# Performance work log

Measured on AMD Instinct MI355X. Metric: run time of the kernel, lower is better.

## Reference

```python
import jax, jax.numpy as jnp
import numpy as np

EPS_N = 1e-12   # F.normalize eps
LN_EPS = 1e-5   # LayerNorm eps
N_NODES = 20000
NODES_PER_GRAPH = 200
DEG = 8
N_EDGES = N_NODES * DEG
F_NODE = 36
F_EDGE = 10
HID = 128
HEAD = 8
DK = HID // HEAD
G = N_NODES // NODES_PER_GRAPH


def l2norm(x):
    n = jnp.sqrt(jnp.sum(x * x, axis=-1, keepdims=True))
    return x / jnp.maximum(n, EPS_N)


def layer_norm(x, g, b):
    m = jnp.mean(x, axis=-1, keepdims=True)
    v = jnp.mean((x - m) ** 2, axis=-1, keepdims=True)
    return (x - m) / jnp.sqrt(v + LN_EPS) * g + b


def seg_softmax(e, idx, n):
    m = jax.ops.segment_max(e, idx, num_segments=n)
    ex = jnp.exp(e - m[idx])
    s = jax.ops.segment_sum(ex, idx, num_segments=n)
    return ex / s[idx]


def sfe_conv(x, src, dst, eattr, We, Wq, Wk, Wv, Wo, bo, g, b):
    # x: [N, in], src/dst: [Ef] (self loops included), eattr: [Ef, F_EDGE]
    n = x.shape[0]
    emb = l2norm(eattr @ We)                  # edge_encoder + F.normalize
    xj = x[src] + emb                          # source node + edge embedding
    q = (xj @ Wq).reshape(-1, HEAD, DK)
    ksum = (x[dst] @ Wk).reshape(-1, HEAD, DK).sum(axis=1)  # sum over k-heads (matmul+sum in source)
    v = (xj @ Wv).reshape(-1, HEAD, DK)
    energy = jnp.einsum('ehd,ed->eh', q, ksum) / jnp.sqrt(jnp.float32(HID))
    att = seg_softmax(energy, dst, n)          # segment softmax over target nodes, per head
    msg = (v * att[:, :, None]).reshape(-1, HID)
    agg = jax.ops.segment_sum(msg, dst, num_segments=n)
    y = layer_norm(agg @ Wo + bo, g, b)        # update(): out_norm(out_linear(.))
    return layer_norm(y, g, b)                 # forward() applies out_norm again


def setup_inputs():
    key = jax.random.key(0)
    ks = jax.random.split(key, 16)
    x = jax.random.normal(ks[0], (N_NODES, F_NODE), jnp.float32)
    edge_attr = jax.random.uniform(ks[1], (N_EDGES, F_EDGE), jnp.float32)
    src = jnp.repeat(jnp.arange(N_NODES), DEG)
    base = src - src % NODES_PER_GRAPH
    off = jax.random.randint(ks[2], (N_EDGES,), 1, NODES_PER_GRAPH)
    dst = base + (src % NODES_PER_GRAPH + off) % NODES_PER_GRAPH  # same-graph, no self loops
    edge_index = jnp.stack([src, dst]).astype(jnp.int64)
    batch = (jnp.arange(N_NODES) // NODES_PER_GRAPH).astype(jnp.int64)
    interface_pos = jnp.arange(0, N_NODES, 2, dtype=jnp.int64)
    s = lambda k, sh: jax.random.normal(k, sh, jnp.float32) * 0.05
    return dict(
        x=x, edge_attr=edge_attr,
        c0_We=s(ks[3], (F_EDGE, F_NODE)), c0_Wq=s(ks[4], (F_NODE, HID)),
        c0_Wk=s(ks[5], (F_NODE, HID)), c0_Wv=s(ks[6], (F_NODE, HID)),
        c0_Wo=s(ks[7], (HID, HID)), c0_bo=jnp.zeros((HID,), jnp.float32),
        c0_g=jnp.ones((HID,), jnp.float32), c0_b=jnp.zeros((HID,), jnp.float32),
        cs_We=s(ks[8], (2, F_EDGE, HID)), cs_Wq=s(ks[9], (2, HID, HID)),
        cs_Wk=s(ks[10], (2, HID, HID)), cs_Wv=s(ks[11], (2, HID, HID)),
        cs_Wo=s(ks[12], (2, HID, HID)), cs_bo=jnp.zeros((2, HID), jnp.float32),
        cs_g=jnp.ones((2, HID), jnp.float32), cs_b=jnp.zeros((2, HID), jnp.float32),
        gate=s(ks[13], (HID,)), W1=s(ks[14], (HID, HID // 2)),
        b1=jnp.zeros((HID // 2,), jnp.float32), W2=s(ks[15], (HID // 2, 1)),
        b2=jnp.zeros((1,), jnp.float32),
        edge_index=edge_index, batch=batch, interface_pos=interface_pos,
        graph_num=G)


def reference(x, edge_attr, c0_We, c0_Wq, c0_Wk, c0_Wv, c0_Wo, c0_bo, c0_g, c0_b,
              cs_We, cs_Wq, cs_Wk, cs_Wv, cs_Wo, cs_bo, cs_g, cs_b,
              gate, W1, b1, W2, b2, edge_index, batch, interface_pos, graph_num):
    n = x.shape[0]
    loops = jnp.arange(n)
    src = jnp.concatenate([edge_index[0], loops])
    dst = jnp.concatenate([edge_index[1], loops])
    ea = jnp.concatenate([l2norm(edge_attr),
                          jnp.zeros((n, edge_attr.shape[1]), edge_attr.dtype)])
    h = l2norm(x)
    h = jnp.tanh(sfe_conv(h, src, dst, ea, c0_We, c0_Wq, c0_Wk, c0_Wv, c0_Wo, c0_bo, c0_g, c0_b))
    for i in range(cs_We.shape[0]):
        h = jnp.tanh(sfe_conv(h, src, dst, ea, cs_We[i], cs_Wq[i], cs_Wk[i], cs_Wv[i],
                              cs_Wo[i], cs_bo[i], cs_g[i], cs_b[i]))
    # global self-attention pooling over interface nodes, per graph
    xi = h[interface_pos]
    bi = batch[interface_pos]
    att = seg_softmax(xi @ gate, bi, graph_num)
    pooled = jax.ops.segment_sum(att[:, None] * xi, bi, num_segments=graph_num)  # [G, HID]
    out = jnp.tanh(pooled @ W1 + b1)
    return jax.nn.sigmoid(out @ W2 + b2)  # [G, 1]
```

## Files before the change

### kernel.cpp

```cpp
#include <hip/hip_runtime.h>
#include <math.h>

#define HID 128
#define HEAD 8
#define DK 16
#define FEDGE 10
#define FNODE 36
#define ESCALE 0.08838834764831845f
#define CH 32

typedef float f32x4v __attribute__((ext_vector_type(4)));
typedef short bf16x8 __attribute__((ext_vector_type(8)));

struct PackArgs {
  const float* src[8];
  unsigned short* dst[8];
  int fin[8];
  int kt[8];
  int blk_off[8];
};

struct PrepArgs {
  const float* We[3];
  const float* Wq[3];
  const float* Wk[3];
  const float* Wv[3];
  float* C[3];
  float* WeWv[3];
  float* Gram[3];
  float* Wksum[3];
  int fin[3];
};

__device__ __forceinline__ void fma4(float4& z, float s, const float4& w) {
  z.x += s * w.x;
  z.y += s * w.y;
  z.z += s * w.z;
  z.w += s * w.w;
}

__device__ __forceinline__ unsigned short f2bf(float f) {
  unsigned int u = __float_as_uint(f);
  u += 0x7fffu + ((u >> 16) & 1u);
  return (unsigned short)(u >> 16);
}

__device__ __forceinline__ void store_bf8(unsigned short* p, float4 a, float4 b) {
  uint4 u;
  u.x = (unsigned)f2bf(a.x) | ((unsigned)f2bf(a.y) << 16);
  u.y = (unsigned)f2bf(a.z) | ((unsigned)f2bf(a.w) << 16);
  u.z = (unsigned)f2bf(b.x) | ((unsigned)f2bf(b.y) << 16);
  u.w = (unsigned)f2bf(b.z) | ((unsigned)f2bf(b.w) << 16);
  *(uint4*)p = u;
}

__global__ void k_zero_i(int* __restrict__ p, int n) {
  int i = blockIdx.x * 256 + threadIdx.x;
  if (i < n) p[i] = 0;
}

__global__ void k_count(const int* __restrict__ ei, int E, int* __restrict__ cnt) {
  int e = blockIdx.x * 256 + threadIdx.x;
  if (e >= E) return;
  atomicAdd(&cnt[ei[E + e]], 1);
}

__global__ __launch_bounds__(1024) void k_scan(const int* __restrict__ cnt, int* __restrict__ off,
                                               int* __restrict__ cur, int* __restrict__ scsr_s,
                                               int n, int total) {
  __shared__ int s[1024];
  int t = threadIdx.x;
  const int C = (n + 1023) / 1024;
  int local[32];
  int base = t * C;
  int sum = 0;
  for (int j = 0; j < C; ++j) {
    int i = base + j;
    int v = (i < n) ? cnt[i] : 0;
    local[j] = sum;
    sum += v;
  }
  s[t] = sum;
  __syncthreads();
  for (int dd = 1; dd < 1024; dd <<= 1) {
    int v = (t >= dd) ? s[t - dd] : 0;
    __syncthreads();
    s[t] += v;
    __syncthreads();
  }
  int excl = (t == 0) ? 0 : s[t - 1];
  for (int j = 0; j < C; ++j) {
    int i = base + j;
    if (i < n) {
      int o = excl + local[j];
      off[i] = o;
      cur[i] = o;
      scsr_s[o + i] = i;
    }
  }
  if (t == 0) off[n] = total;
}

__global__ void k_fill(const int* __restrict__ ei, int E, int* __restrict__ cur,
                       int* __restrict__ scsr_s, int* __restrict__ pmap) {
  int e = blockIdx.x * 256 + threadIdx.x;
  if (e >= E) return;
  int t = ei[E + e];
  int pos = atomicAdd(&cur[t], 1) + t + 1;
  pmap[e] = pos;
  scsr_s[pos] = ei[e];
}

__global__ __launch_bounds__(128) void k_wprep3(PrepArgs a) {
  int l = blockIdx.x / FEDGE, t = blockIdx.x - l * FEDGE;
  int d = threadIdx.x;
  int fin = a.fin[l];
  const float* We = a.We[l];
  const float* Wq = a.Wq[l];
  const float* Wk = a.Wk[l];
  const float* Wv = a.Wv[l];
  __shared__ float sw[HID];
  if (d < fin) sw[d] = We[t * fin + d];
  __syncthreads();
  float c = 0.f, wv = 0.f;
  for (int i = 0; i < fin; ++i) {
    c += sw[i] * Wq[i * HID + d];
    wv += sw[i] * Wv[i * HID + d];
  }
  a.C[l][t * HID + d] = c;
  a.WeWv[l][t * HID + d] = wv;
  if (d < FEDGE) {
    float g = 0.f;
    for (int i = 0; i < fin; ++i) g += sw[i] * We[d * fin + i];
    a.Gram[l][t * FEDGE + d] = g;
  }
  for (int r = t; r < fin; r += FEDGE) {
    if (d < DK) {
      float s = 0.f;
#pragma unroll
      for (int hh = 0; hh < HEAD; ++hh) s += Wk[r * HID + hh * DK + d];
      a.Wksum[l][r * DK + d] = s;
    }
  }
}

__global__ __launch_bounds__(64) void k_wpack8(PackArgs pa) {
  int b = blockIdx.x, lane = threadIdx.x;
  int m = 0;
#pragma unroll
  for (int i = 1; i < 8; ++i) m += (b >= pa.blk_off[i]);
  int local = b - pa.blk_off[m];
  int KT = pa.kt[m];
  int ct = local / KT, kt = local - ct * KT;
  const float* W = pa.src[m];
  int fin = pa.fin[m];
  int col = ct * 16 + (lane & 15);
  int kbase = kt * 32 + (lane >> 4) * 8;
  float v[8];
#pragma unroll
  for (int j = 0; j < 8; ++j) {
    int k = kbase + j;
    v[j] = (k < fin) ? W[k * HID + col] : 0.f;
  }
  store_bf8(pa.dst[m] + (size_t)local * 512 + lane * 8, make_float4(v[0], v[1], v[2], v[3]),
            make_float4(v[4], v[5], v[6], v[7]));
}

__global__ void k_l2e_sea(const float* __restrict__ eattr, const int* __restrict__ pmap,
                          const float* __restrict__ Gram3, float* __restrict__ sea3, int E,
                          int ET) {
  int e = blockIdx.x * 256 + threadIdx.x;
  if (e >= E) return;
  float a[FEDGE];
  float ss = 0.f;
  for (int i = 0; i < FEDGE; ++i) {
    a[i] = eattr[(size_t)e * FEDGE + i];
    ss += a[i] * a[i];
  }
  float s0 = 1.f / fmaxf(sqrtf(ss), 1e-12f);
  for (int i = 0; i < FEDGE; ++i) a[i] *= s0;
  int pos = pmap[e];
  for (int l = 0; l < 3; ++l) {
    const float* G = Gram3 + l * FEDGE * FEDGE;
    float gp = 0.f;
#pragma unroll
    for (int j = 0; j < FEDGE; ++j) {
      float t = 0.f;
#pragma unroll
      for (int u = 0; u < FEDGE; ++u) t += G[j * FEDGE + u] * a[u];
      gp += t * a[j];
    }
    float scl = 1.f / fmaxf(sqrtf(gp), 1e-12f);
    float* sp = sea3 + (size_t)l * ET * FEDGE + (size_t)pos * FEDGE;
#pragma unroll
    for (int u = 0; u < FEDGE; ++u) sp[u] = scl * a[u];
  }
}

__global__ __launch_bounds__(256) void k1_l2x(
    const float* __restrict__ x, const unsigned short* __restrict__ qpack,
    const unsigned short* __restrict__ vpack, const float* __restrict__ Wksum,
    const float* __restrict__ C, const int* __restrict__ off, float* __restrict__ qx,
    float* __restrict__ kb, float* __restrict__ vxb, float* __restrict__ Mout,
    float* __restrict__ energy_csr, int N) {
  const int fin = FNODE;
  int d = threadIdx.x;
  int n0 = blockIdx.x * 16;
  int nb = min(16, N - n0);
  __shared__ __align__(16) float sx[16][40];
  __shared__ __align__(16) unsigned short afrag[2][64][8];
  __shared__ float sk[16][DK];
  {
    int col = d & 127, h2 = d >> 7;
#pragma unroll
    for (int rr = 0; rr < 8; ++rr) {
      int r = h2 * 8 + rr;
      if (col < fin) sx[r][col] = (r < nb) ? x[(size_t)(n0 + r) * fin + col] : 0.f;
    }
  }
  __syncthreads();
  int grp = d >> 4, j16 = d & 15;
  {
    float ssq = 0.f;
    for (int i = j16; i < fin; i += 16) ssq += sx[grp][i] * sx[grp][i];
#pragma unroll
    for (int o = 8; o; o >>= 1) ssq += __shfl_xor(ssq, o, 16);
    float scl = 1.f / fmaxf(sqrtf(ssq), 1e-12f);
    for (int i = j16; i < fin; i += 16) sx[grp][i] *= scl;
  }
  __syncthreads();
  int lane = d & 63, wvid = d >> 6;
  if (d < 128) {
    int kt = d >> 6;
    int m = lane & 15, k0 = kt * 32 + (lane >> 4) * 8;
    float v[8];
#pragma unroll
    for (int j = 0; j < 8; ++j) {
      int k = k0 + j;
      v[j] = (k < fin) ? sx[m][k] : 0.f;
    }
    store_bf8(&afrag[kt][lane][0], make_float4(v[0], v[1], v[2], v[3]),
              make_float4(v[4], v[5], v[6], v[7]));
  }
  {
    float kk = 0.f;
    for (int i = 0; i < fin; ++i) kk += sx[grp][i] * Wksum[i * DK + j16];
    sk[grp][j16] = kk;
    if (grp < nb) kb[(size_t)(n0 + grp) * DK + j16] = kk;
  }
  __syncthreads();
  int colD = lane & 15, quad = lane >> 4;
#pragma unroll
  for (int t = 0; t < 4; ++t) {
    int g = wvid * 4 + t;
    int mat = g >> 3, ct = g & 7;
    const unsigned short* P = mat ? vpack : qpack;
    f32x4v acc = {0.f, 0.f, 0.f, 0.f};
#pragma unroll
    for (int kt = 0; kt < 2; ++kt) {
      bf16x8 a = *(const bf16x8*)&afrag[kt][lane][0];
      bf16x8 b = *(const bf16x8*)(P + ((size_t)(ct * 2 + kt) * 64 + lane) * 8);
      acc = __builtin_amdgcn_mfma_f32_16x16x32_bf16(a, b, acc, 0, 0, 0);
    }
    float* out = mat ? vxb : qx;
#pragma unroll
    for (int reg = 0; reg < 4; ++reg) {
      int node = quad * 4 + reg;
      if (node < nb) out[(size_t)(n0 + node) * HID + ct * 16 + colD] = acc[reg];
    }
  }
  __syncthreads();
  if (d < 128) {
    int n = d >> 3, h = d & 7;
    if (n < nb) {
      const float* qp = qx + (size_t)(n0 + n) * HID + h * DK;
      float e = 0.f;
#pragma unroll
      for (int j = 0; j < DK; ++j) e += qp[j] * sk[n][j];
      int nn = n0 + n;
      energy_csr[(size_t)(off[nn] + nn) * HEAD + h] = e * ESCALE;
    }
  }
  if (d < HEAD * FEDGE) {
    int hh = d / FEDGE, tt = d - hh * FEDGE;
    float crow[16];
    *(float4*)&crow[0] = *(const float4*)&C[tt * HID + hh * DK + 0];
    *(float4*)&crow[4] = *(const float4*)&C[tt * HID + hh * DK + 4];
    *(float4*)&crow[8] = *(const float4*)&C[tt * HID + hh * DK + 8];
    *(float4*)&crow[12] = *(const float4*)&C[tt * HID + hh * DK + 12];
    for (int r = 0; r < nb; ++r) {
      float m = 0.f;
#pragma unroll
      for (int j = 0; j < DK; ++j) m += sk[r][j] * crow[j];
      Mout[((size_t)(n0 + r) * HEAD + hh) * 16 + tt] = m;
    }
  }
}

__global__ __launch_bounds__(256) void k_post_k1(
    const float* agg, const unsigned short* __restrict__ opack, const float* __restrict__ bo,
    const float* __restrict__ gg, const float* __restrict__ bb,
    const unsigned short* __restrict__ qpack, const unsigned short* __restrict__ vpack,
    const float* __restrict__ Wksum, const float* __restrict__ C, const int* __restrict__ off,
    float* qx, float* __restrict__ kb, float* __restrict__ vxb, float* __restrict__ Mout,
    float* __restrict__ energy_csr, int N) {
  int d = threadIdx.x;
  int n0 = blockIdx.x * 16;
  int nb = min(16, N - n0);
  __shared__ __align__(16) unsigned short afrag[4][64][8];
  __shared__ __align__(16) float sz[16][132];
  __shared__ __align__(16) unsigned short hfrag[4][64][8];
  __shared__ float sk[16][DK];
  int lane = d & 63, wvid = d >> 6;
  {
    int kt = wvid;
    int m = lane & 15, k0 = kt * 32 + (lane >> 4) * 8;
    const float* p = agg + (size_t)(n0 + m) * HID + k0;
    float4 x0 = *(const float4*)p;
    float4 x1 = *(const float4*)(p + 4);
    store_bf8(&afrag[kt][lane][0], x0, x1);
  }
  __syncthreads();
  int colD = lane & 15, quad = lane >> 4;
  {
    int ct0 = wvid * 2, ct1 = wvid * 2 + 1;
    float bias0 = bo[ct0 * 16 + colD], bias1 = bo[ct1 * 16 + colD];
    f32x4v acc0 = {bias0, bias0, bias0, bias0};
    f32x4v acc1 = {bias1, bias1, bias1, bias1};
#pragma unroll
    for (int kt = 0; kt < 4; ++kt) {
      bf16x8 a = *(const bf16x8*)&afrag[kt][lane][0];
      bf16x8 b0 = *(const bf16x8*)(opack + ((size_t)(ct0 * 4 + kt) * 64 + lane) * 8);
      bf16x8 b1 = *(const bf16x8*)(opack + ((size_t)(ct1 * 4 + kt) * 64 + lane) * 8);
      acc0 = __builtin_amdgcn_mfma_f32_16x16x32_bf16(a, b0, acc0, 0, 0, 0);
      acc1 = __builtin_amdgcn_mfma_f32_16x16x32_bf16(a, b1, acc1, 0, 0, 0);
    }
#pragma unroll
    for (int reg = 0; reg < 4; ++reg) {
      int node = quad * 4 + reg;
      sz[node][ct0 * 16 + colD] = acc0[reg];
      sz[node][ct1 * 16 + colD] = acc1[reg];
    }
  }
  __syncthreads();
  {
    int c4 = d & 31, rs = d >> 5;
    int col0 = c4 * 4, r0 = rs * 2;
    float4 zA = *(const float4*)&sz[r0][col0];
    float4 zB = *(const float4*)&sz[r0 + 1][col0];
    float4 g4 = *(const float4*)&gg[col0];
    float4 b4 = *(const float4*)&bb[col0];
#pragma unroll
    for (int pass = 0; pass < 2; ++pass) {
      float sA = zA.x + zA.y + zA.z + zA.w;
      float qA = zA.x * zA.x + zA.y * zA.y + zA.z * zA.z + zA.w * zA.w;
      float sB = zB.x + zB.y + zB.z + zB.w;
      float qB = zB.x * zB.x + zB.y * zB.y + zB.z * zB.z + zB.w * zB.w;
#pragma unroll
      for (int o = 16; o; o >>= 1) {
        sA += __shfl_xor(sA, o, 32);
        qA += __shfl_xor(qA, o, 32);
        sB += __shfl_xor(sB, o, 32);
        qB += __shfl_xor(qB, o, 32);
      }
      float mA = sA * (1.f / 128.f);
      float iA = rsqrtf(fmaxf(qA * (1.f / 128.f) - mA * mA, 0.f) + 1e-5f);
      float mB = sB * (1.f / 128.f);
      float iB = rsqrtf(fmaxf(qB * (1.f / 128.f) - mB * mB, 0.f) + 1e-5f);
      zA.x = (zA.x - mA) * iA * g4.x + b4.x;
      zA.y = (zA.y - mA) * iA * g4.y + b4.y;
      zA.z = (zA.z - mA) * iA * g4.z + b4.z;
      zA.w = (zA.w - mA) * iA * g4.w + b4.w;
      zB.x = (zB.x - mB) * iB * g4.x + b4.x;
      zB.y = (zB.y - mB) * iB * g4.y + b4.y;
      zB.z = (zB.z - mB) * iB * g4.z + b4.z;
      zB.w = (zB.w - mB) * iB * g4.w + b4.w;
    }
    zA.x = tanhf(zA.x);
    zA.y = tanhf(zA.y);
    zA.z = tanhf(zA.z);
    zA.w = tanhf(zA.w);
    zB.x = tanhf(zB.x);
    zB.y = tanhf(zB.y);
    zB.z = tanhf(zB.z);
    zB.w = tanhf(zB.w);
    *(float4*)&sz[r0][col0] = zA;
    *(float4*)&sz[r0 + 1][col0] = zB;
    int chunk = col0 >> 5, qd = (col0 >> 3) & 3, eo = col0 & 7;
    unsigned int loA = (unsigned)f2bf(zA.x) | ((unsigned)f2bf(zA.y) << 16);
    unsigned int hiA = (unsigned)f2bf(zA.z) | ((unsigned)f2bf(zA.w) << 16);
    unsigned int loB = (unsigned)f2bf(zB.x) | ((unsigned)f2bf(zB.y) << 16);
    unsigned int hiB = (unsigned)f2bf(zB.z) | ((unsigned)f2bf(zB.w) << 16);
    unsigned short* pA = &hfrag[chunk][(r0 & 15) + qd * 16][eo];
    unsigned short* pB = &hfrag[chunk][((r0 + 1) & 15) + qd * 16][eo];
    *(unsigned int*)pA = loA;
    *(unsigned int*)(pA + 2) = hiA;
    *(unsigned int*)pB = loB;
    *(unsigned int*)(pB + 2) = hiB;
  }
  __syncthreads();
#pragma unroll
  for (int t = 0; t < 4; ++t) {
    int g = wvid * 4 + t;
    int mat = g >> 3, ct = g & 7;
    const unsigned short* P = mat ? vpack : qpack;
    f32x4v acc = {0.f, 0.f, 0.f, 0.f};
#pragma unroll
    for (int kt = 0; kt < 4; ++kt) {
      bf16x8 a = *(const bf16x8*)&hfrag[kt][lane][0];
      bf16x8 b = *(const bf16x8*)(P + ((size_t)(ct * 4 + kt) * 64 + lane) * 8);
      acc = __builtin_amdgcn_mfma_f32_16x16x32_bf16(a, b, acc, 0, 0, 0);
    }
    float* out = mat ? vxb : qx;
#pragma unroll
    for (int reg = 0; reg < 4; ++reg) {
      int node = quad * 4 + reg;
      if (node < nb) out[(size_t)(n0 + node) * HID + ct * 16 + colD] = acc[reg];
    }
  }
  int grp = d >> 4, j16 = d & 15;
  {
    float kk = 0.f;
    for (int i = 0; i < HID; ++i) kk += sz[grp][i] * Wksum[i * DK + j16];
    sk[grp][j16] = kk;
    if (grp < nb) kb[(size_t)(n0 + grp) * DK + j16] = kk;
  }
  __syncthreads();
  if (d < 128) {
    int n = d >> 3, h = d & 7;
    if (n < nb) {
      const float* qp = qx + (size_t)(n0 + n) * HID + h * DK;
      float e = 0.f;
#pragma unroll
      for (int j = 0; j < DK; ++j) e += qp[j] * sk[n][j];
      int nn = n0 + n;
      energy_csr[(size_t)(off[nn] + nn) * HEAD + h] = e * ESCALE;
    }
  }
  if (d < HEAD * FEDGE) {
    int hh = d / FEDGE, tt = d - hh * FEDGE;
    float crow[16];
    *(float4*)&crow[0] = *(const float4*)&C[tt * HID + hh * DK + 0];
    *(float4*)&crow[4] = *(const float4*)&C[tt * HID + hh * DK + 4];
    *(float4*)&crow[8] = *(const float4*)&C[tt * HID + hh * DK + 8];
    *(float4*)&crow[12] = *(const float4*)&C[tt * HID + hh * DK + 12];
    for (int r = 0; r < nb; ++r) {
      float m = 0.f;
#pragma unroll
      for (int j = 0; j < DK; ++j) m += sk[r][j] * crow[j];
      Mout[((size_t)(n0 + r) * HEAD + hh) * 16 + tt] = m;
    }
  }
}

__global__ __launch_bounds__(256) void k2_eh(const int* __restrict__ ei, int E,
                                             const float* __restrict__ qx,
                                             const float* __restrict__ kb,
                                             const float* __restrict__ Mbuf,
                                             const float* __restrict__ sea,
                                             const int* __restrict__ pmap,
                                             float* __restrict__ energy_csr) {
  int gid = blockIdx.x * 256 + threadIdx.x;
  if (gid >= E * HEAD) return;
  int e = gid >> 3, h = gid & 7;
  int s = ei[e], t = ei[E + e];
  int pos = pmap[e];
  const float4* qp = (const float4*)(qx + (size_t)s * HID + h * DK);
  const float4* kp = (const float4*)(kb + (size_t)t * DK);
  float en = 0.f;
#pragma unroll
  for (int j = 0; j < 4; ++j) {
    float4 q4 = qp[j], k4 = kp[j];
    en += q4.x * k4.x + q4.y * k4.y + q4.z * k4.z + q4.w * k4.w;
  }
  const float* Mp = Mbuf + ((size_t)t * HEAD + h) * 16;
  const float* sp = sea + (size_t)pos * FEDGE;
#pragma unroll
  for (int u = 0; u < FEDGE; ++u) en += Mp[u] * sp[u];
  energy_csr[(size_t)pos * HEAD + h] = en * ESCALE;
}

__global__ __launch_bounds__(128) void k3_gather(
    const int* __restrict__ off, const int* __restrict__ scsr_s,
    const float* __restrict__ energy_csr, const float* __restrict__ sea,
    const float* __restrict__ vxb, const float* __restrict__ WeWv, float* agg, int N) {
  int b = blockIdx.x;
  int n = ((N & 7) == 0) ? ((b & 7) * (N >> 3) + (b >> 3)) : b;
  int d = threadIdx.x;
  int j16 = d & 15, hd = d >> 4;
  __shared__ float sen[CH * 8];
  __shared__ float ssea[CH * 10];
  __shared__ int ss[CH];
  __shared__ float sT[HEAD * FEDGE];
  int base = off[n] + n;
  int cnt = off[n + 1] + n + 1 - base;
  bool doT = (j16 < FEDGE);
  float m = -1e30f, l = 0.f, accv = 0.f, T = 0.f;
  for (int c0 = 0; c0 < cnt; c0 += CH) {
    int cc = min(CH, cnt - c0);
    for (int idx = d; idx < cc * 8; idx += 128)
      sen[idx] = energy_csr[(size_t)(base + c0) * 8 + idx];
    for (int idx = d; idx < cc * 10; idx += 128)
      ssea[idx] = sea[(size_t)(base + c0) * 10 + idx];
    if (d < cc) ss[d] = scsr_s[base + c0 + d];
    __syncthreads();
    float mloc = -1e30f;
    for (int o = 0; o < cc; ++o) mloc = fmaxf(mloc, sen[o * 8 + hd]);
    float mnew = fmaxf(m, mloc);
    float alpha = __expf(m - mnew);
    l *= alpha;
    accv *= alpha;
    T *= alpha;
#pragma unroll 2
    for (int o = 0; o < cc; ++o) {
      int s = ss[o];
      float p = __expf(sen[o * 8 + hd] - mnew);
      l += p;
      accv += p * vxb[(size_t)s * HID + d];
      if (doT && (c0 + o) > 0) T += p * ssea[o * 10 + j16];
    }
    m = mnew;
    __syncthreads();
  }
  float inv = 1.f / l;
  if (doT) sT[hd * FEDGE + j16] = T * inv;
  __syncthreads();
  float y = accv * inv;
#pragma unroll
  for (int t = 0; t < FEDGE; ++t) y += sT[hd * FEDGE + t] * WeWv[t * HID + d];
  agg[(size_t)n * HID + d] = y;
}

__global__ __launch_bounds__(256) void k_post(const float* agg, const float* __restrict__ Wo,
                                              const float* __restrict__ bo,
                                              const float* __restrict__ gg,
                                              const float* __restrict__ bb,
                                              float* __restrict__ hout, int N) {
  int d = threadIdx.x;
  int n0 = blockIdx.x * 16;
  int nb = min(16, N - n0);
  __shared__ __align__(16) float sh[16][132];
  {
    int col = d & 127, h2 = d >> 7;
#pragma unroll
    for (int rr = 0; rr < 8; ++rr) {
      int r = h2 * 8 + rr;
      sh[r][col] = (r < nb) ? agg[(size_t)(n0 + r) * HID + col] : 0.f;
    }
  }
  __syncthreads();
  int c4 = d & 31, rs = d >> 5;
  int col0 = c4 * 4, r0 = rs * 2;
  float4 bv = *(const float4*)&bo[col0];
  float4 zA = bv, zB = bv;
  for (int k4 = 0; k4 < 32; ++k4) {
    float4 w0 = *(const float4*)&Wo[(k4 * 4 + 0) * HID + col0];
    float4 w1 = *(const float4*)&Wo[(k4 * 4 + 1) * HID + col0];
    float4 w2 = *(const float4*)&Wo[(k4 * 4 + 2) * HID + col0];
    float4 w3 = *(const float4*)&Wo[(k4 * 4 + 3) * HID + col0];
    float4 a0 = *(const float4*)&sh[r0][k4 * 4];
    float4 a1 = *(const float4*)&sh[r0 + 1][k4 * 4];
    fma4(zA, a0.x, w0);
    fma4(zA, a0.y, w1);
    fma4(zA, a0.z, w2);
    fma4(zA, a0.w, w3);
    fma4(zB, a1.x, w0);
    fma4(zB, a1.y, w1);
    fma4(zB, a1.z, w2);
    fma4(zB, a1.w, w3);
  }
  float4 g4 = *(const float4*)&gg[col0];
  float4 b4 = *(const float4*)&bb[col0];
#pragma unroll
  for (int pass = 0; pass < 2; ++pass) {
    float sA = zA.x + zA.y + zA.z + zA.w;
    float qA = zA.x * zA.x + zA.y * zA.y + zA.z * zA.z + zA.w * zA.w;
    float sB = zB.x + zB.y + zB.z + zB.w;
    float qB = zB.x * zB.x + zB.y * zB.y + zB.z * zB.z + zB.w * zB.w;
#pragma unroll
    for (int o = 16; o; o >>= 1) {
      sA += __shfl_xor(sA, o, 32);
      qA += __shfl_xor(qA, o, 32);
      sB += __shfl_xor(sB, o, 32);
      qB += __shfl_xor(qB, o, 32);
    }
    float mA = sA * (1.f / 128.f);
    float iA = rsqrtf(fmaxf(qA * (1.f / 128.f) - mA * mA, 0.f) + 1e-5f);
    float mB = sB * (1.f / 128.f);
    float iB = rsqrtf(fmaxf(qB * (1.f / 128.f) - mB * mB, 0.f) + 1e-5f);
    zA.x = (zA.x - mA) * iA * g4.x + b4.x;
    zA.y = (zA.y - mA) * iA * g4.y + b4.y;
    zA.z = (zA.z - mA) * iA * g4.z + b4.z;
    zA.w = (zA.w - mA) * iA * g4.w + b4.w;
    zB.x = (zB.x - mB) * iB * g4.x + b4.x;
    zB.y = (zB.y - mB) * iB * g4.y + b4.y;
    zB.z = (zB.z - mB) * iB * g4.z + b4.z;
    zB.w = (zB.w - mB) * iB * g4.w + b4.w;
  }
  if (r0 < nb) {
    float4 o0 = make_float4(tanhf(zA.x), tanhf(zA.y), tanhf(zA.z), tanhf(zA.w));
    *(float4*)&hout[(size_t)(n0 + r0) * HID + col0] = o0;
  }
  if (r0 + 1 < nb) {
    float4 o1 = make_float4(tanhf(zB.x), tanhf(zB.y), tanhf(zB.z), tanhf(zB.w));
    *(float4*)&hout[(size_t)(n0 + r0 + 1) * HID + col0] = o1;
  }
}

__global__ __launch_bounds__(128) void k4_pool(const float* __restrict__ h,
                                               const int* __restrict__ ipos,
                                               const float* __restrict__ gate,
                                               const float* __restrict__ W1,
                                               const float* __restrict__ b1,
                                               const float* __restrict__ W2,
                                               const float* __restrict__ b2,
                                               float* __restrict__ out, int per_g) {
  int g = blockIdx.x, d = threadIdx.x;
  __shared__ int snode[128];
  __shared__ float satt[128], spool[HID], so[64], sv[2];
  if (d < per_g) snode[d] = ipos[g * per_g + d];
  __syncthreads();
  float sc = -1e30f;
  if (d < per_g) {
    float s = 0.f;
    int node = snode[d];
    for (int i = 0; i < HID; ++i) s += h[(size_t)node * HID + i] * gate[i];
    sc = s;
  }
  satt[d] = sc;
  __syncthreads();
  if (d == 0) {
    float m = -1e30f;
    for (int i = 0; i < per_g; ++i) m = fmaxf(m, satt[i]);
    sv[0] = m;
  }
  __syncthreads();
  float m = sv[0];
  float ex = (d < per_g) ? __expf(sc - m) : 0.f;
  satt[d] = ex;
  __syncthreads();
  if (d == 0) {
    float su = 0.f;
    for (int i = 0; i < per_g; ++i) su += satt[i];
    sv[1] = 1.f / su;
  }
  __syncthreads();
  float inv = sv[1];
  float p = 0.f;
  for (int i = 0; i < per_g; ++i) p += satt[i] * h[(size_t)snode[i] * HID + d];
  spool[d] = p * inv;
  __syncthreads();
  if (d < 64) {
    float o = b1[d];
    for (int i = 0; i < HID; ++i) o += spool[i] * W1[i * 64 + d];
    so[d] = tanhf(o);
  }
  __syncthreads();
  if (d == 0) {
    float z = b2[0];
    for (int i = 0; i < 64; ++i) z += so[i] * W2[i];
    out[g] = 1.f / (1.f + __expf(-z));
  }
}

extern "C" void kernel_launch(void* const* d_in, const int* in_sizes, int n_in, void* d_out,
                              int out_size, void* d_ws, size_t ws_size, hipStream_t stream) {
  const float* x = (const float*)d_in[0];
  const float* eattr = (const float*)d_in[1];
  const float* c0_We = (const float*)d_in[2];
  const float* c0_Wq = (const float*)d_in[3];
  const float* c0_Wk = (const float*)d_in[4];
  const float* c0_Wv = (const float*)d_in[5];
  const float* c0_Wo = (const float*)d_in[6];
  const float* c0_bo = (const float*)d_in[7];
  const float* c0_g = (const float*)d_in[8];
  const float* c0_b = (const float*)d_in[9];
  const float* cs_We = (const float*)d_in[10];
  const float* cs_Wq = (const float*)d_in[11];
  const float* cs_Wk = (const float*)d_in[12];
  const float* cs_Wv = (const float*)d_in[13];
  const float* cs_Wo = (const float*)d_in[14];
  const float* cs_bo = (const float*)d_in[15];
  const float* cs_g = (const float*)d_in[16];
  const float* cs_b = (const float*)d_in[17];
  const float* gate = (const float*)d_in[18];
  const float* W1 = (const float*)d_in[19];
  const float* b1 = (const float*)d_in[20];
  const float* W2 = (const float*)d_in[21];
  const float* b2 = (const float*)d_in[22];
  const int* ei = (const int*)d_in[23];
  const int* ipos = (const int*)d_in[25];

  int N = in_sizes[0] / FNODE;
  int E = in_sizes[1] / FEDGE;
  int G = out_size;
  int per_g = in_sizes[25] / G;
  int ET = E + N;

  float* w = (float*)d_ws;
  float* hB = w;         w += (size_t)N * HID;
  float* qx = w;         w += (size_t)N * HID;
  float* kb = w;         w += (size_t)N * DK;
  float* vx = w;         w += (size_t)N * HID;
  float* Mbuf = w;       w += (size_t)N * HEAD * 16;
  float* energy_csr = w; w += (size_t)ET * HEAD;
  float* sea3 = w;       w += (size_t)3 * ET * FEDGE;
  float* C3 = w;         w += 3 * FEDGE * HID;
  float* WeWv3 = w;      w += 3 * FEDGE * HID;
  float* Gram3 = w;      w += 3 * FEDGE * FEDGE;
  float* Wksum3 = w;     w += 3 * HID * DK;
  unsigned short* qp3 = (unsigned short*)w;  w += 3 * 16384 / 2;
  unsigned short* vp3 = (unsigned short*)w;  w += 3 * 16384 / 2;
  unsigned short* op2 = (unsigned short*)w;  w += 2 * 16384 / 2;
  int* cnt = (int*)w;
  int* off = cnt + (N + 1);
  int* cur = off + (N + 1);
  int* scsr_s = cur + N;
  int* pmap = scsr_s + ET;

  const float* Ws[3][8] = {
      {c0_We, c0_Wq, c0_Wk, c0_Wv, c0_Wo, c0_bo, c0_g, c0_b},
      {cs_We, cs_Wq, cs_Wk, cs_Wv, cs_Wo, cs_bo, cs_g, cs_b},
      {cs_We + FEDGE * HID, cs_Wq + HID * HID, cs_Wk + HID * HID, cs_Wv + HID * HID,
       cs_Wo + HID * HID, cs_bo + HID, cs_g + HID, cs_b + HID}};
  int fins[3] = {FNODE, HID, HID};

  PrepArgs prep;
  for (int l = 0; l < 3; ++l) {
    prep.We[l] = Ws[l][0];
    prep.Wq[l] = Ws[l][1];
    prep.Wk[l] = Ws[l][2];
    prep.Wv[l] = Ws[l][3];
    prep.C[l] = C3 + l * FEDGE * HID;
    prep.WeWv[l] = WeWv3 + l * FEDGE * HID;
    prep.Gram[l] = Gram3 + l * FEDGE * FEDGE;
    prep.Wksum[l] = Wksum3 + l * HID * DK;
    prep.fin[l] = fins[l];
  }
  k_wprep3<<<3 * FEDGE, 128, 0, stream>>>(prep);

  PackArgs pa;
  {
    const float* srcs[8] = {Ws[0][1], Ws[0][3], Ws[1][1], Ws[1][3],
                            Ws[2][1], Ws[2][3], Ws[0][4], Ws[1][4]};
    unsigned short* dsts[8] = {qp3, vp3, qp3 + 16384, vp3 + 16384, qp3 + 2 * 16384,
                               vp3 + 2 * 16384, op2, op2 + 16384};
    int fns[8] = {FNODE, FNODE, HID, HID, HID, HID, HID, HID};
    int kts[8] = {2, 2, 4, 4, 4, 4, 4, 4};
    int offb = 0;
    for (int i = 0; i < 8; ++i) {
      pa.src[i] = srcs[i];
      pa.dst[i] = dsts[i];
      pa.fin[i] = fns[i];
      pa.kt[i] = kts[i];
      pa.blk_off[i] = offb;
      offb += 8 * kts[i];
    }
    k_wpack8<<<offb, 64, 0, stream>>>(pa);
  }

  k_zero_i<<<(N + 1 + 255) / 256, 256, 0, stream>>>(cnt, N + 1);
  k_count<<<(E + 255) / 256, 256, 0, stream>>>(ei, E, cnt);
  k_scan<<<1, 1024, 0, stream>>>(cnt, off, cur, scsr_s, N, E);
  k_fill<<<(E + 255) / 256, 256, 0, stream>>>(ei, E, cur, scsr_s, pmap);
  k_l2e_sea<<<(E + 255) / 256, 256, 0, stream>>>(eattr, pmap, Gram3, sea3, E, ET);

  k1_l2x<<<(N + 15) / 16, 256, 0, stream>>>(x, qp3, vp3, Wksum3, C3, off, qx, kb, vx, Mbuf,
                                            energy_csr, N);
  for (int l = 0; l < 3; ++l) {
    const float* sea_l = sea3 + (size_t)l * ET * FEDGE;
    k2_eh<<<(E * HEAD + 255) / 256, 256, 0, stream>>>(ei, E, qx, kb, Mbuf, sea_l, pmap,
                                                      energy_csr);
    k3_gather<<<N, 128, 0, stream>>>(off, scsr_s, energy_csr, sea_l, vx,
                                     WeWv3 + l * FEDGE * HID, qx , N);
    if (l < 2) {
      k_post_k1<<<(N + 15) / 16, 256, 0, stream>>>(
          qx , op2 + l * 16384, Ws[l][5], Ws[l][6], Ws[l][7], qp3 + (l + 1) * 16384,
          vp3 + (l + 1) * 16384, Wksum3 + (l + 1) * HID * DK, C3 + (l + 1) * FEDGE * HID, off, qx,
          kb, vx, Mbuf, energy_csr, N);
    } else {
      k_post<<<(N + 15) / 16, 256, 0, stream>>>(qx , Ws[l][4], Ws[l][5], Ws[l][6],
                                                Ws[l][7], hB, N);
    }
  }
  k4_pool<<<G, 128, 0, stream>>>(hB, ipos, gate, W1, b1, W2, b2, (float*)d_out, per_g);
}
```

Measured before the change: 429.0 us.

## Fuse edge energy computation into gather kernel and drop k2_eh pass

Removes the separate per-edge energy kernel and its energy_csr buffer. The gather kernel now computes each incoming edge's attention energy on the fly, from the source node's q row, the target's k row and M vector, and the edge attribute, using a 16-lane shuffle reduction. A separate aggregation buffer is added because qx is still read during the gather and can no longer be overwritten in place. This saves one kernel launch per layer and a round trip of energies through global memory, at the cost of serial per-edge reductions and an extra synchronisation inside the gather loop.

```diff
diff --git a/kernel.cpp b/kernel.cpp
--- a/kernel.cpp
+++ b/kernel.cpp
@@ -200,9 +200,8 @@
 __global__ __launch_bounds__(256) void k1_l2x(
     const float* __restrict__ x, const unsigned short* __restrict__ qpack,
     const unsigned short* __restrict__ vpack, const float* __restrict__ Wksum,
-    const float* __restrict__ C, const int* __restrict__ off, float* __restrict__ qx,
-    float* __restrict__ kb, float* __restrict__ vxb, float* __restrict__ Mout,
-    float* __restrict__ energy_csr, int N) {
+    const float* __restrict__ C, float* __restrict__ qx, float* __restrict__ kb,
+    float* __restrict__ vxb, float* __restrict__ Mout, int N) {
   const int fin = FNODE;
   int d = threadIdx.x;
   int n0 = blockIdx.x * 16;
@@ -267,18 +266,6 @@
     for (int reg = 0; reg < 4; ++reg) {
       int node = quad * 4 + reg;
       if (node < nb) out[(size_t)(n0 + node) * HID + ct * 16 + colD] = acc[reg];
-    }
-  }
-  __syncthreads();
-  if (d < 128) {
-    int n = d >> 3, h = d & 7;
-    if (n < nb) {
-      const float* qp = qx + (size_t)(n0 + n) * HID + h * DK;
-      float e = 0.f;
-#pragma unroll
-      for (int j = 0; j < DK; ++j) e += qp[j] * sk[n][j];
-      int nn = n0 + n;
-      energy_csr[(size_t)(off[nn] + nn) * HEAD + h] = e * ESCALE;
     }
   }
   if (d < HEAD * FEDGE) {
@@ -298,12 +285,11 @@
 }
 
 __global__ __launch_bounds__(256) void k_post_k1(
-    const float* agg, const unsigned short* __restrict__ opack, const float* __restrict__ bo,
-    const float* __restrict__ gg, const float* __restrict__ bb,
+    const float* __restrict__ agg, const unsigned short* __restrict__ opack,
+    const float* __restrict__ bo, const float* __restrict__ gg, const float* __restrict__ bb,
     const unsigned short* __restrict__ qpack, const unsigned short* __restrict__ vpack,
-    const float* __restrict__ Wksum, const float* __restrict__ C, const int* __restrict__ off,
-    float* qx, float* __restrict__ kb, float* __restrict__ vxb, float* __restrict__ Mout,
-    float* __restrict__ energy_csr, int N) {
+    const float* __restrict__ Wksum, const float* __restrict__ C, float* __restrict__ qx,
+    float* __restrict__ kb, float* __restrict__ vxb, float* __restrict__ Mout, int N) {
   int d = threadIdx.x;
   int n0 = blockIdx.x * 16;
   int nb = min(16, N - n0);
@@ -426,17 +412,6 @@
     if (grp < nb) kb[(size_t)(n0 + grp) * DK + j16] = kk;
   }
   __syncthreads();
-  if (d < 128) {
-    int n = d >> 3, h = d & 7;
-    if (n < nb) {
-      const float* qp = qx + (size_t)(n0 + n) * HID + h * DK;
-      float e = 0.f;
-#pragma unroll
-      for (int j = 0; j < DK; ++j) e += qp[j] * sk[n][j];
-      int nn = n0 + n;
-      energy_csr[(size_t)(off[nn] + nn) * HEAD + h] = e * ESCALE;
-    }
-  }
   if (d < HEAD * FEDGE) {
     int hh = d / FEDGE, tt = d - hh * FEDGE;
     float crow[16];
@@ -453,37 +428,11 @@
   }
 }
 
-__global__ __launch_bounds__(256) void k2_eh(const int* __restrict__ ei, int E,
-                                             const float* __restrict__ qx,
-                                             const float* __restrict__ kb,
-                                             const float* __restrict__ Mbuf,
-                                             const float* __restrict__ sea,
-                                             const int* __restrict__ pmap,
-                                             float* __restrict__ energy_csr) {
-  int gid = blockIdx.x * 256 + threadIdx.x;
-  if (gid >= E * HEAD) return;
-  int e = gid >> 3, h = gid & 7;
-  int s = ei[e], t = ei[E + e];
-  int pos = pmap[e];
-  const float4* qp = (const float4*)(qx + (size_t)s * HID + h * DK);
-  const float4* kp = (const float4*)(kb + (size_t)t * DK);
-  float en = 0.f;
-#pragma unroll
-  for (int j = 0; j < 4; ++j) {
-    float4 q4 = qp[j], k4 = kp[j];
-    en += q4.x * k4.x + q4.y * k4.y + q4.z * k4.z + q4.w * k4.w;
-  }
-  const float* Mp = Mbuf + ((size_t)t * HEAD + h) * 16;
-  const float* sp = sea + (size_t)pos * FEDGE;
-#pragma unroll
-  for (int u = 0; u < FEDGE; ++u) en += Mp[u] * sp[u];
-  energy_csr[(size_t)pos * HEAD + h] = en * ESCALE;
-}
-
 __global__ __launch_bounds__(128) void k3_gather(
-    const int* __restrict__ off, const int* __restrict__ scsr_s,
-    const float* __restrict__ energy_csr, const float* __restrict__ sea,
-    const float* __restrict__ vxb, const float* __restrict__ WeWv, float* agg, int N) {
+    const int* __restrict__ off, const int* __restrict__ scsr_s, const float* __restrict__ sea,
+    const float* __restrict__ qx, const float* __restrict__ kb, const float* __restrict__ Mbuf,
+    const float* __restrict__ vxb, const float* __restrict__ WeWv, float* __restrict__ agg,
+    int N) {
   int b = blockIdx.x;
   int n = ((N & 7) == 0) ? ((b & 7) * (N >> 3) + (b >> 3)) : b;
   int d = threadIdx.x;
@@ -494,15 +443,24 @@
   __shared__ float sT[HEAD * FEDGE];
   int base = off[n] + n;
   int cnt = off[n + 1] + n + 1 - base;
+  float kreg = kb[(size_t)n * DK + j16];
+  float Mreg = Mbuf[(size_t)n * 128 + d];
   bool doT = (j16 < FEDGE);
   float m = -1e30f, l = 0.f, accv = 0.f, T = 0.f;
   for (int c0 = 0; c0 < cnt; c0 += CH) {
     int cc = min(CH, cnt - c0);
-    for (int idx = d; idx < cc * 8; idx += 128)
-      sen[idx] = energy_csr[(size_t)(base + c0) * 8 + idx];
     for (int idx = d; idx < cc * 10; idx += 128)
       ssea[idx] = sea[(size_t)(base + c0) * 10 + idx];
     if (d < cc) ss[d] = scsr_s[base + c0 + d];
+    __syncthreads();
+    for (int o = 0; o < cc; ++o) {
+      int s = ss[o];
+      float part = qx[(size_t)s * HID + d] * kreg;
+      if (doT && (c0 + o) > 0) part += Mreg * ssea[o * 10 + j16];
+#pragma unroll
+      for (int w = 8; w; w >>= 1) part += __shfl_xor(part, w, 16);
+      if (j16 == 0) sen[o * 8 + hd] = part * ESCALE;
+    }
     __syncthreads();
     float mloc = -1e30f;
     for (int o = 0; o < cc; ++o) mloc = fmaxf(mloc, sen[o * 8 + hd]);
@@ -531,7 +489,8 @@
   agg[(size_t)n * HID + d] = y;
 }
 
-__global__ __launch_bounds__(256) void k_post(const float* agg, const float* __restrict__ Wo,
+__global__ __launch_bounds__(256) void k_post(const float* __restrict__ agg,
+                                              const float* __restrict__ Wo,
                                               const float* __restrict__ bo,
                                               const float* __restrict__ gg,
                                               const float* __restrict__ bb,
@@ -700,10 +659,10 @@
   float* w = (float*)d_ws;
   float* hB = w;         w += (size_t)N * HID;
   float* qx = w;         w += (size_t)N * HID;
+  float* aggb = w;       w += (size_t)N * HID;
   float* kb = w;         w += (size_t)N * DK;
   float* vx = w;         w += (size_t)N * HID;
   float* Mbuf = w;       w += (size_t)N * HEAD * 16;
-  float* energy_csr = w; w += (size_t)ET * HEAD;
   float* sea3 = w;       w += (size_t)3 * ET * FEDGE;
   float* C3 = w;         w += 3 * FEDGE * HID;
   float* WeWv3 = w;      w += 3 * FEDGE * HID;
@@ -765,22 +724,19 @@
   k_fill<<<(E + 255) / 256, 256, 0, stream>>>(ei, E, cur, scsr_s, pmap);
   k_l2e_sea<<<(E + 255) / 256, 256, 0, stream>>>(eattr, pmap, Gram3, sea3, E, ET);
 
-  k1_l2x<<<(N + 15) / 16, 256, 0, stream>>>(x, qp3, vp3, Wksum3, C3, off, qx, kb, vx, Mbuf,
-                                            energy_csr, N);
+  k1_l2x<<<(N + 15) / 16, 256, 0, stream>>>(x, qp3, vp3, Wksum3, C3, qx, kb, vx, Mbuf, N);
   for (int l = 0; l < 3; ++l) {
     const float* sea_l = sea3 + (size_t)l * ET * FEDGE;
-    k2_eh<<<(E * HEAD + 255) / 256, 256, 0, stream>>>(ei, E, qx, kb, Mbuf, sea_l, pmap,
-                                                      energy_csr);
-    k3_gather<<<N, 128, 0, stream>>>(off, scsr_s, energy_csr, sea_l, vx,
-                                     WeWv3 + l * FEDGE * HID, qx , N);
+    k3_gather<<<N, 128, 0, stream>>>(off, scsr_s, sea_l, qx, kb, Mbuf, vx,
+                                     WeWv3 + l * FEDGE * HID, aggb, N);
     if (l < 2) {
       k_post_k1<<<(N + 15) / 16, 256, 0, stream>>>(
-          qx , op2 + l * 16384, Ws[l][5], Ws[l][6], Ws[l][7], qp3 + (l + 1) * 16384,
-          vp3 + (l + 1) * 16384, Wksum3 + (l + 1) * HID * DK, C3 + (l + 1) * FEDGE * HID, off, qx,
-          kb, vx, Mbuf, energy_csr, N);
+          aggb, op2 + l * 16384, Ws[l][5], Ws[l][6], Ws[l][7], qp3 + (l + 1) * 16384,
+          vp3 + (l + 1) * 16384, Wksum3 + (l + 1) * HID * DK, C3 + (l + 1) * FEDGE * HID, qx, kb,
+          vx, Mbuf, N);
     } else {
-      k_post<<<(N + 15) / 16, 256, 0, stream>>>(qx , Ws[l][4], Ws[l][5], Ws[l][6],
-                                                Ws[l][7], hB, N);
+      k_post<<<(N + 15) / 16, 256, 0, stream>>>(aggb, Ws[l][4], Ws[l][5], Ws[l][6], Ws[l][7], hB,
+                                                N);
     }
   }
   k4_pool<<<G, 128, 0, stream>>>(hB, ipos, gate, W1, b1, W2, b2, (float*)d_out, per_g);
```

Measured after the change: 447.3 us. 4.3% more time.
